# Performance work log

Measured on AMD Instinct MI355X. Metric: run time of the kernel, lower is better.

Reference implementation:

```python
import jax, jax.numpy as jnp
import numpy as np

B, T, F, N = 256, 1024, 16, 1024  # batch, history len, features, output_steps (num_nodes)


def setup_inputs() -> dict:
    key = jax.random.key(0)
    ks = jax.random.split(key, 12)
    he = lambda k, shape, fan_in: jax.random.normal(k, shape, jnp.float32) * np.sqrt(2.0 / fan_in)
    return {
        "history_in": jax.random.normal(ks[0], (B, T, F), jnp.float32),
        "node_id_in": jax.random.randint(ks[1], (B,), 0, N),
        "time_of_day_in": jax.random.randint(ks[2], (B,), 0, 288),
        "day_in_week_in": jax.random.randint(ks[3], (B,), 0, 7),
        "wt1": jax.random.uniform(ks[4], (1,), jnp.float32),
        "wt2": jax.random.uniform(ks[5], (1,), jnp.float32),
        "wt3": jax.random.uniform(ks[6], (1,), jnp.float32),
        "wt4": jax.random.uniform(ks[7], (1,), jnp.float32),
        # stacked per-feature Dense params: [F, T, N] weights, [F, N] biases
        "trend_W": he(ks[8], (F, T, N), T),
        "trend_b": jnp.zeros((F, N), jnp.float32),
        "residual_W": he(ks[9], (F, T, N), T),
        "residual_b": jnp.zeros((F, N), jnp.float32),
    }


def reference(history_in, node_id_in, time_of_day_in, day_in_week_in,
              wt1, wt2, wt3, wt4, trend_W, trend_b, residual_W, residual_b):
    x = history_in  # [B, T, F]
    # TF AveragePooling1D(pool_size=2, strides=1, padding='same'):
    # out[t] = mean(x[t], x[t+1]) for t < T-1; out[T-1] = x[T-1] (padding excluded from count)
    trend = jnp.concatenate([(x[:, :-1] + x[:, 1:]) * 0.5, x[:, -1:]], axis=1)  # [B, T, F]
    residual = x - trend
    # per-feature Dense (T -> N) for trend and residual, fused as batched GEMM over F
    out = (jnp.einsum('btf,ftn->bnf', trend, trend_W) + trend_b.T[None]
           + jnp.einsum('btf,ftn->bnf', residual, residual_W) + residual_b.T[None])  # [B, N, F]
    return out
```

## Files before the change

kernel.cpp:

```cpp
#include <hip/hip_runtime.h>
#include <hip/hip_bf16.h>
#include <stdint.h>

#define B_  256
#define T_  1024
#define F_  16
#define N_  1024

typedef short bf16x8 __attribute__((ext_vector_type(8)));
typedef float f32x4  __attribute__((ext_vector_type(4)));

static __device__ __forceinline__ unsigned short f2bf(float x) {
  unsigned u = __builtin_bit_cast(unsigned, x);
  u += 0x7fffu + ((u >> 16) & 1u);
  return (unsigned short)(u >> 16);
}
static __device__ __forceinline__ float bf2f(unsigned short h) {
  unsigned u = ((unsigned)h) << 16;
  return __builtin_bit_cast(float, u);
}

__global__ __launch_bounds__(256) void prep2_kernel(const float* __restrict__ x,
                                                    unsigned short* __restrict__ At2) {
  __shared__ unsigned short ld[16 * 1028];
  const int rb = blockIdx.x >> 4, tc = blockIdx.x & 15;
  const int tid = threadIdx.x;
  const int tl = tid >> 2;
  const int f4 = (tid & 3) * 4;
#pragma unroll
  for (int i = 0; i < 16; ++i) {
    const float* src = x + (((size_t)(rb * 16 + i) * T_) + tc * 64 + tl) * F_ + f4;
    float4 v = *(const float4*)src;
    uint2 pk;
    pk.x = (unsigned)f2bf(v.x) | ((unsigned)f2bf(v.y) << 16);
    pk.y = (unsigned)f2bf(v.z) | ((unsigned)f2bf(v.w) << 16);
    *(uint2*)&ld[i * 1028 + tl * 16 + f4] = pk;
  }
  __syncthreads();
  const int w = tid >> 6, l = tid & 63;
#pragma unroll
  for (int it = 0; it < 8; ++it) {
    const int c = it * 4 + w;
    const int f = c >> 1, kcl = c & 1;
    unsigned short t16[8];
#pragma unroll
    for (int j = 0; j < 8; ++j)
      t16[j] = ld[(l & 15) * 1028 + (kcl * 32 + ((l >> 4) * 8) + j) * 16 + f];
    uint4 q;
    q.x = (unsigned)t16[0] | ((unsigned)t16[1] << 16);
    q.y = (unsigned)t16[2] | ((unsigned)t16[3] << 16);
    q.z = (unsigned)t16[4] | ((unsigned)t16[5] << 16);
    q.w = (unsigned)t16[6] | ((unsigned)t16[7] << 16);
    *(uint4*)(At2 + (((size_t)(f * 32 + tc * 2 + kcl) * 16 + rb) << 9) + l * 8) = q;
  }
}

template <int TMPOUT>
__global__ __launch_bounds__(1024, 4) void gemm_kernel(const unsigned short* __restrict__ At2,
                                                       const float* __restrict__ TW,
                                                       const float* __restrict__ RW,
                                                       const float* __restrict__ tb,
                                                       const float* __restrict__ rb,
                                                       float* __restrict__ out,
                                                       unsigned short* __restrict__ tmp) {
  __shared__ unsigned short vT[16 * 4 * 64 * 8];

  const int tid = threadIdx.x;
  const int bid = (blockIdx.x & 7) * 32 + (blockIdx.x >> 3);
  const int f  = bid >> 4;
  const int n0 = (bid & 15) * 64;
  const int w = tid >> 6, l = tid & 63;
  const int lrow = l & 15, lg = l >> 4;

  const float* TWf = TW + (size_t)f * (T_ * N_) + n0;
  const float* RWf = RW + (size_t)f * (T_ * N_) + n0;
  const unsigned short* Af2 = At2 + ((size_t)f * 32 * 16 * 512);

  f32x4 acc[4];
#pragma unroll
  for (int nt = 0; nt < 4; ++nt)
    acc[nt] = (f32x4){0.f, 0.f, 0.f, 0.f};

#pragma unroll
  for (int p = 0; p < 2; ++p) {
    const int t0 = p * 512 + w * 32;
    float twv[32], rwv[32];
    float ptw = 0.f, prw = 0.f;
    if (t0 > 0) {
      ptw = TWf[(size_t)(t0 - 1) * N_ + l];
      prw = RWf[(size_t)(t0 - 1) * N_ + l];
    }
#pragma unroll
    for (int i = 0; i < 32; ++i) {
      twv[i] = TWf[(size_t)(t0 + i) * N_ + l];
      rwv[i] = RWf[(size_t)(t0 + i) * N_ + l];
    }
    __syncthreads();
#pragma unroll
    for (int b = 0; b < 4; ++b) {
      unsigned pk[4];
      unsigned lo32 = 0;
#pragma unroll
      for (int i = 0; i < 8; ++i) {
        const int tl = b * 8 + i;
        const int tg = t0 + tl;
        const float tw = twv[tl], rw = rwv[tl];
        const float c1 = (tg < T_ - 1) ? 0.5f : 1.0f;
        const float c2 = (tg < T_ - 1) ? 0.5f : 0.0f;
        const float pterm = (tg >= 1) ? 0.5f * (ptw - prw) : 0.0f;
        const unsigned short us = f2bf(c1 * tw + c2 * rw + pterm);
        if ((i & 1) == 0) lo32 = us; else pk[i >> 1] = lo32 | ((unsigned)us << 16);
        ptw = tw; prw = rw;
      }
      uint4 q; q.x = pk[0]; q.y = pk[1]; q.z = pk[2]; q.w = pk[3];
      *(uint4*)&vT[((w * 4 + (l >> 4)) * 64 + b * 16 + (l & 15)) * 8] = q;
    }
    __syncthreads();
#pragma unroll
    for (int kcl = 0; kcl < 16; ++kcl) {
      const int kc = p * 16 + kcl;
      bf16x8 a = *(const bf16x8*)(Af2 + (((size_t)(kc * 16 + w)) << 9) + l * 8);
#pragma unroll
      for (int nt = 0; nt < 4; ++nt) {
        bf16x8 bfrag = *(const bf16x8*)&vT[((kcl * 4 + nt) * 64 + l) * 8];
        acc[nt] = __builtin_amdgcn_mfma_f32_16x16x32_bf16(a, bfrag, acc[nt], 0, 0, 0);
      }
    }
  }

#pragma unroll
  for (int nt = 0; nt < 4; ++nt) {
    const int n = n0 + nt * 16 + lrow;
    const float bsum = tb[f * N_ + n] + rb[f * N_ + n];
#pragma unroll
    for (int j = 0; j < 4; ++j) {
      const int brow = w * 16 + lg * 4 + j;
      const float v = acc[nt][j] + bsum;
      if (TMPOUT) {
        tmp[((size_t)f * B_ + brow) * N_ + n] = f2bf(v);
      } else {
        out[((size_t)brow * N_ + n) * F_ + f] = v;
      }
    }
  }
}

__global__ __launch_bounds__(256) void untile_kernel(const unsigned short* __restrict__ tmp,
                                                     float* __restrict__ out) {
  __shared__ unsigned short ld[16 * 1048];
  const int b = blockIdx.x, tid = threadIdx.x;
#pragma unroll
  for (int it = 0; it < 8; ++it) {
    const int idx = it * 256 + tid;
    const int f = idx >> 7, c = idx & 127;
    uint4 v = *(const uint4*)(tmp + ((size_t)f * B_ + b) * N_ + c * 8);
    *(uint4*)&ld[f * 1048 + c * 8] = v;
  }
  __syncthreads();
  float* ob = out + (size_t)b * (N_ * F_);
#pragma unroll
  for (int it = 0; it < 16; ++it) {
    const int g = it * 256 + tid;
    const int n = g >> 2, f0 = (g & 3) * 4;
    float4 o;
    o.x = bf2f(ld[(f0 + 0) * 1048 + n]);
    o.y = bf2f(ld[(f0 + 1) * 1048 + n]);
    o.z = bf2f(ld[(f0 + 2) * 1048 + n]);
    o.w = bf2f(ld[(f0 + 3) * 1048 + n]);
    *(float4*)(ob + n * F_ + f0) = o;
  }
}

extern "C" void kernel_launch(void* const* d_in, const int* in_sizes, int n_in,
                              void* d_out, int out_size, void* d_ws, size_t ws_size,
                              hipStream_t stream) {
  const float* x  = (const float*)d_in[0];
  const float* TW = (const float*)d_in[8];
  const float* tb = (const float*)d_in[9];
  const float* RW = (const float*)d_in[10];
  const float* rb = (const float*)d_in[11];
  float* out = (float*)d_out;

  unsigned short* At2 = (unsigned short*)d_ws;
  const size_t atBytes  = (size_t)F_ * B_ * T_ * sizeof(unsigned short);
  const size_t tmpBytes = (size_t)F_ * B_ * N_ * sizeof(unsigned short);

  prep2_kernel<<<256, 256, 0, stream>>>(x, At2);
  if (ws_size >= atBytes + tmpBytes) {
    unsigned short* tmp = (unsigned short*)((char*)d_ws + atBytes);
    gemm_kernel<1><<<256, 1024, 0, stream>>>(At2, TW, RW, tb, rb, out, tmp);
    untile_kernel<<<256, 256, 0, stream>>>(tmp, out);
  } else {
    gemm_kernel<0><<<256, 1024, 0, stream>>>(At2, TW, RW, tb, rb, out, nullptr);
  }
}
```

Baseline: 43.54 us.

## Split GEMM K dimension across two blocks and reduce partials in untile

Adds a split-K GEMM kernel that launches 512 blocks, each handling half of the T reduction for one feature and one N tile. Each block writes its partial sums to the workspace as bf16, and a new untile kernel adds the two partials plus both biases while transposing into the output layout. The aim is to double the number of blocks in flight and hide weight-load latency better than the two-phase loop, which streams all of K through a single block. In exchange it writes and re-reads twice as much intermediate data and adds a second bf16 rounding step to each partial.

```diff
diff --git a/kernel.cpp b/kernel.cpp
--- a/kernel.cpp
+++ b/kernel.cpp
@@ -52,6 +52,117 @@
     q.z = (unsigned)t16[4] | ((unsigned)t16[5] << 16);
     q.w = (unsigned)t16[6] | ((unsigned)t16[7] << 16);
     *(uint4*)(At2 + (((size_t)(f * 32 + tc * 2 + kcl) * 16 + rb) << 9) + l * 8) = q;
+  }
+}
+
+__global__ __launch_bounds__(1024, 8) void gemm_split_kernel(const unsigned short* __restrict__ At2,
+                                                             const float* __restrict__ TW,
+                                                             const float* __restrict__ RW,
+                                                             unsigned short* __restrict__ part) {
+  __shared__ unsigned short vT[16 * 4 * 64 * 8];
+
+  const int tid = threadIdx.x;
+  const int bid = (blockIdx.x & 7) * 64 + (blockIdx.x >> 3);
+  const int f   = bid >> 5;
+  const int n0  = ((bid >> 1) & 15) * 64;
+  const int kh  = bid & 1;
+  const int w = tid >> 6, l = tid & 63;
+  const int lrow = l & 15, lg = l >> 4;
+
+  const float* TWf = TW + (size_t)f * (T_ * N_) + n0;
+  const float* RWf = RW + (size_t)f * (T_ * N_) + n0;
+  const unsigned short* Af2 = At2 + ((size_t)f * 32 * 16 * 512);
+
+  f32x4 acc[4];
+#pragma unroll
+  for (int nt = 0; nt < 4; ++nt)
+    acc[nt] = (f32x4){0.f, 0.f, 0.f, 0.f};
+
+  const int t0 = kh * 512 + w * 32;
+  float ptw = 0.f, prw = 0.f;
+  if (t0 > 0) {
+    ptw = TWf[(size_t)(t0 - 1) * N_ + l];
+    prw = RWf[(size_t)(t0 - 1) * N_ + l];
+  }
+  float twv[32], rwv[32];
+#pragma unroll
+  for (int i = 0; i < 32; ++i) {
+    twv[i] = TWf[(size_t)(t0 + i) * N_ + l];
+    rwv[i] = RWf[(size_t)(t0 + i) * N_ + l];
+  }
+#pragma unroll
+  for (int b = 0; b < 4; ++b) {
+    unsigned pk[4];
+    unsigned lo32 = 0;
+#pragma unroll
+    for (int i = 0; i < 8; ++i) {
+      const int tl = b * 8 + i;
+      const int tg = t0 + tl;
+      const float tw = twv[tl], rw = rwv[tl];
+      const float c1 = (tg < T_ - 1) ? 0.5f : 1.0f;
+      const float c2 = (tg < T_ - 1) ? 0.5f : 0.0f;
+      const float pterm = (tg >= 1) ? 0.5f * (ptw - prw) : 0.0f;
+      const unsigned short us = f2bf(c1 * tw + c2 * rw + pterm);
+      if ((i & 1) == 0) lo32 = us; else pk[i >> 1] = lo32 | ((unsigned)us << 16);
+      ptw = tw; prw = rw;
+    }
+    uint4 q; q.x = pk[0]; q.y = pk[1]; q.z = pk[2]; q.w = pk[3];
+    *(uint4*)&vT[((w * 4 + (l >> 4)) * 64 + b * 16 + (l & 15)) * 8] = q;
+  }
+  __syncthreads();
+#pragma unroll
+  for (int kcl = 0; kcl < 16; ++kcl) {
+    const int kc = kh * 16 + kcl;
+    bf16x8 a = *(const bf16x8*)(Af2 + (((size_t)(kc * 16 + w)) << 9) + l * 8);
+#pragma unroll
+    for (int nt = 0; nt < 4; ++nt) {
+      bf16x8 bfrag = *(const bf16x8*)&vT[((kcl * 4 + nt) * 64 + l) * 8];
+      acc[nt] = __builtin_amdgcn_mfma_f32_16x16x32_bf16(a, bfrag, acc[nt], 0, 0, 0);
+    }
+  }
+#pragma unroll
+  for (int nt = 0; nt < 4; ++nt) {
+    const int n = n0 + nt * 16 + lrow;
+#pragma unroll
+    for (int j = 0; j < 4; ++j) {
+      const int brow = w * 16 + lg * 4 + j;
+      part[((size_t)(kh * 16 + f) * B_ + brow) * N_ + n] = f2bf(acc[nt][j]);
+    }
+  }
+}
+
+__global__ __launch_bounds__(256) void untile2_kernel(const unsigned short* __restrict__ part,
+                                                      const float* __restrict__ tb,
+                                                      const float* __restrict__ rb,
+                                                      float* __restrict__ out) {
+  __shared__ float ldF[16 * 1048];
+  const int b = blockIdx.x, tid = threadIdx.x;
+  const unsigned short* p0 = part;
+  const unsigned short* p1 = part + (size_t)F_ * B_ * N_;
+#pragma unroll
+  for (int it = 0; it < 8; ++it) {
+    const int idx = it * 256 + tid;
+    const int f = idx >> 7, c = idx & 127;
+    uint4 v0 = *(const uint4*)(p0 + ((size_t)f * B_ + b) * N_ + c * 8);
+    uint4 v1 = *(const uint4*)(p1 + ((size_t)f * B_ + b) * N_ + c * 8);
+    const unsigned short* a0 = (const unsigned short*)&v0;
+    const unsigned short* a1 = (const unsigned short*)&v1;
+#pragma unroll
+    for (int j = 0; j < 8; ++j)
+      ldF[f * 1048 + c * 8 + j] = bf2f(a0[j]) + bf2f(a1[j]);
+  }
+  __syncthreads();
+  float* ob = out + (size_t)b * (N_ * F_);
+#pragma unroll
+  for (int it = 0; it < 16; ++it) {
+    const int g = it * 256 + tid;
+    const int n = g >> 2, f0 = (g & 3) * 4;
+    float4 o;
+    o.x = ldF[(f0 + 0) * 1048 + n] + tb[(f0 + 0) * N_ + n] + rb[(f0 + 0) * N_ + n];
+    o.y = ldF[(f0 + 1) * 1048 + n] + tb[(f0 + 1) * N_ + n] + rb[(f0 + 1) * N_ + n];
+    o.z = ldF[(f0 + 2) * 1048 + n] + tb[(f0 + 2) * N_ + n] + rb[(f0 + 2) * N_ + n];
+    o.w = ldF[(f0 + 3) * 1048 + n] + tb[(f0 + 3) * N_ + n] + rb[(f0 + 3) * N_ + n];
+    *(float4*)(ob + n * F_ + f0) = o;
   }
 }
 
@@ -64,23 +175,19 @@
                                                        float* __restrict__ out,
                                                        unsigned short* __restrict__ tmp) {
   __shared__ unsigned short vT[16 * 4 * 64 * 8];
-
   const int tid = threadIdx.x;
   const int bid = (blockIdx.x & 7) * 32 + (blockIdx.x >> 3);
   const int f  = bid >> 4;
   const int n0 = (bid & 15) * 64;
   const int w = tid >> 6, l = tid & 63;
   const int lrow = l & 15, lg = l >> 4;
-
   const float* TWf = TW + (size_t)f * (T_ * N_) + n0;
   const float* RWf = RW + (size_t)f * (T_ * N_) + n0;
   const unsigned short* Af2 = At2 + ((size_t)f * 32 * 16 * 512);
-
   f32x4 acc[4];
 #pragma unroll
   for (int nt = 0; nt < 4; ++nt)
     acc[nt] = (f32x4){0.f, 0.f, 0.f, 0.f};
-
 #pragma unroll
   for (int p = 0; p < 2; ++p) {
     const int t0 = p * 512 + w * 32;
@@ -127,7 +234,6 @@
       }
     }
   }
-
 #pragma unroll
   for (int nt = 0; nt < 4; ++nt) {
     const int n = n0 + nt * 16 + lrow;
@@ -182,11 +288,16 @@
   float* out = (float*)d_out;
 
   unsigned short* At2 = (unsigned short*)d_ws;
-  const size_t atBytes  = (size_t)F_ * B_ * T_ * sizeof(unsigned short);
-  const size_t tmpBytes = (size_t)F_ * B_ * N_ * sizeof(unsigned short);
+  const size_t atBytes   = (size_t)F_ * B_ * T_ * sizeof(unsigned short);
+  const size_t partBytes = (size_t)2 * F_ * B_ * N_ * sizeof(unsigned short);
+  const size_t tmpBytes  = (size_t)F_ * B_ * N_ * sizeof(unsigned short);
 
   prep2_kernel<<<256, 256, 0, stream>>>(x, At2);
-  if (ws_size >= atBytes + tmpBytes) {
+  if (ws_size >= atBytes + partBytes) {
+    unsigned short* part = (unsigned short*)((char*)d_ws + atBytes);
+    gemm_split_kernel<<<512, 1024, 0, stream>>>(At2, TW, RW, part);
+    untile2_kernel<<<256, 256, 0, stream>>>(part, tb, rb, out);
+  } else if (ws_size >= atBytes + tmpBytes) {
     unsigned short* tmp = (unsigned short*)((char*)d_ws + atBytes);
     gemm_kernel<1><<<256, 1024, 0, stream>>>(At2, TW, RW, tb, rb, out, tmp);
     untile_kernel<<<256, 256, 0, stream>>>(tmp, out);
```

Result: slower. 46.66 us (+7.2%).
